# Kernel tuning notes

Measured on AMD Instinct MI355X. Metric: run time of the kernel, lower is better.

Reference implementation:

```python
import jax, jax.numpy as jnp
import numpy as np

B, L, DIM, H = 2, 2048, 3072, 24
D = DIM // H  # head_dim = 128
EPS = 1e-6


def _rms_norm(x, scale):
    # matches torch RMSNorm: compute in fp32, eps=1e-6, scale of shape [D]
    x32 = x.astype(jnp.float32)
    rrms = jax.lax.rsqrt(jnp.mean(x32 * x32, axis=-1, keepdims=True) + EPS)
    return (x32 * rrms * scale.astype(jnp.float32)).astype(x.dtype)


def _apply_rope(t, pe):
    # t: [B,H,L,D]; pe: [B,1,L,D//2,2,2]
    t_ = t.astype(jnp.float32).reshape(B, H, L, D // 2, 1, 2)
    out = pe[..., 0] * t_[..., 0] + pe[..., 1] * t_[..., 1]  # [B,H,L,D//2,2]
    return out.reshape(B, H, L, D).astype(t.dtype)


def setup_inputs() -> dict:
    key = jax.random.key(0)
    ks = jax.random.split(key, 7)
    x = jax.random.normal(ks[0], (B, L, DIM), jnp.float32)
    pe = jax.random.normal(ks[1], (B, 1, L, D // 2, 2, 2), jnp.float32)
    qkv_w = jax.random.normal(ks[2], (3 * DIM, DIM), jnp.float32) * (DIM ** -0.5)
    proj_w = jax.random.normal(ks[3], (DIM, DIM), jnp.float32) * (DIM ** -0.5)
    proj_b = jnp.zeros((DIM,), jnp.float32)
    q_scale = jnp.ones((D,), jnp.float32)
    k_scale = jnp.ones((D,), jnp.float32)
    return {"x": x, "pe": pe, "qkv_w": qkv_w, "proj_w": proj_w,
            "proj_b": proj_b, "q_scale": q_scale, "k_scale": k_scale}


def reference(x, pe, qkv_w, proj_w, proj_b, q_scale, k_scale):
    # fused QKV projection: [B,L,3*DIM]
    qkv = jnp.einsum('bld,ed->ble', x, qkv_w)
    # 'B L (K H D) -> K B H L D'
    qkv = qkv.reshape(B, L, 3, H, D).transpose(2, 0, 3, 1, 4)
    q, k, v = qkv[0], qkv[1], qkv[2]
    # QK-RMSNorm over head_dim
    q = _rms_norm(q, q_scale)
    k = _rms_norm(k, k_scale)
    # RoPE
    q = _apply_rope(q, pe)
    k = _apply_rope(k, pe)
    # scaled dot-product attention (no mask)
    scores = jnp.einsum('bhqd,bhkd->bhqk', q, k) / jnp.sqrt(jnp.float32(D))
    attn = jax.nn.softmax(scores, axis=-1)
    o = jnp.einsum('bhqk,bhkd->bhqd', attn, v)
    # 'B H L D -> B L (H D)'
    o = o.transpose(0, 2, 1, 3).reshape(B, L, DIM)
    return o @ proj_w.T + proj_b
```

## Files before the change

kernel.cpp:

```cpp
#include <hip/hip_runtime.h>

typedef unsigned short ushort_t;
typedef unsigned short ushort8 __attribute__((ext_vector_type(8)));
typedef __bf16 bf16x8 __attribute__((ext_vector_type(8)));
typedef float f32x4 __attribute__((ext_vector_type(4)));
typedef float f32x16 __attribute__((ext_vector_type(16)));
typedef unsigned uint32x4 __attribute__((ext_vector_type(4)));

#define DEV __device__ __forceinline__

DEV ushort_t f2bf(float f) {
  unsigned u = __builtin_bit_cast(unsigned, f);
  u += 0x7FFFu + ((u >> 16) & 1u);
  return (ushort_t)(u >> 16);
}
DEV float bf2f(ushort_t u) {
  return __builtin_bit_cast(float, ((unsigned)u) << 16);
}
DEV void gload_lds16(const void* g, void* s) {
  __builtin_amdgcn_global_load_lds(
      (__attribute__((address_space(1))) void*)(size_t)g,
      (__attribute__((address_space(3))) void*)(size_t)s, 16, 0, 0);
}
DEV f32x4 mfma_bf16(ushort8 a, ushort8 b, f32x4 c) {
  return __builtin_amdgcn_mfma_f32_16x16x32_bf16(
      __builtin_bit_cast(bf16x8, a), __builtin_bit_cast(bf16x8, b), c, 0, 0, 0);
}
DEV f32x16 mfma32(ushort8 a, ushort8 b, f32x16 c) {
  return __builtin_amdgcn_mfma_f32_32x32x16_bf16(
      __builtin_bit_cast(bf16x8, a), __builtin_bit_cast(bf16x8, b), c, 0, 0, 0);
}
DEV f32x16 zero16() {
  f32x16 z;
#pragma unroll
  for (int i = 0; i < 16; ++i) z[i] = 0.f;
  return z;
}
DEV unsigned cvtpk(float lo, float hi2) {
  unsigned r;
  asm("v_cvt_pk_bf16_f32 %0, %1, %2" : "=v"(r) : "v"(lo), "v"(hi2));
  return r;
}
DEV void swap32(unsigned &x, unsigned &y) {
#if __has_builtin(__builtin_amdgcn_permlane32_swap)
  auto t = __builtin_amdgcn_permlane32_swap(x, y, false, false);
  x = (unsigned)t[0];
  y = (unsigned)t[1];
#else
  unsigned xs = (unsigned)__shfl_xor((int)x, 32, 64);
  unsigned ys = (unsigned)__shfl_xor((int)y, 32, 64);
  bool h = (threadIdx.x & 63) >= 32;
  unsigned nx = h ? ys : x;
  unsigned ny = h ? y : xs;
  x = nx; y = ny;
#endif
}
DEV void barx() {
  asm volatile("" ::: "memory");
  __builtin_amdgcn_s_barrier();
  asm volatile("" ::: "memory");
}
#define GATE_VM2 asm volatile("s_waitcnt vmcnt(2)" ::: "memory")
#define GATE_VM8 asm volatile("s_waitcnt vmcnt(8)" ::: "memory")

__global__ void cast_bf16(const float4* __restrict__ in,
                          ushort4* __restrict__ out, int n4) {
  int stride = gridDim.x * blockDim.x;
  for (int i = blockIdx.x * blockDim.x + threadIdx.x; i < n4; i += stride) {
    float4 v = in[i];
    out[i] = make_ushort4(f2bf(v.x), f2bf(v.y), f2bf(v.z), f2bf(v.w));
  }
}

template <int OUT_BF16, int ADD_BIAS>
__global__ __launch_bounds__(512, 2)
void gemm256(const ushort_t* __restrict__ A, const ushort_t* __restrict__ Bw,
             const float* __restrict__ bias, void* __restrict__ Cp,
             int M, int N, int K) {
  __shared__ ushort_t As[2][256 * 64];
  __shared__ ushort_t Bs[2][256 * 64];
  const int tid = threadIdx.x;
  const int w = tid >> 6, l = tid & 63;
  const int g = l >> 4, r = l & 15;
  const int wm = w >> 2, wn = w & 3;
  const int m0 = blockIdx.y * 256, n0 = blockIdx.x * 256;
  const int NT = K >> 6;
  const int NI = NT >> 1;

  int srow[4], soff[4];
#pragma unroll
  for (int i = 0; i < 4; ++i) {
    int u = i * 512 + tid;
    int row = u >> 3, pc = u & 7;
    srow[i] = row;
    soff[i] = (pc ^ (row & 7)) * 8;
  }

  auto stA = [&](int i, int t, int db) {
    gload_lds16(A + (size_t)(m0 + srow[i]) * K + t * 64 + soff[i],
                As[db] + (i * 512 + w * 64) * 8);
  };
  auto stB = [&](int i, int t, int db) {
    gload_lds16(Bw + (size_t)(n0 + srow[i]) * K + t * 64 + soff[i],
                Bs[db] + (i * 512 + w * 64) * 8);
  };
  auto rdA = [&](int db, int mi, int kk) -> ushort8 {
    int row = wm * 128 + mi * 16 + r;
    return *(const ushort8*)(As[db] + row * 64 + (((kk << 2) + g) ^ (r & 7)) * 8);
  };
  auto rdB = [&](int db, int ni, int kk) -> ushort8 {
    int col = wn * 64 + ni * 16 + r;
    return *(const ushort8*)(Bs[db] + col * 64 + (((kk << 2) + g) ^ (r & 7)) * 8);
  };

  f32x4 acc[8][4];
#pragma unroll
  for (int i = 0; i < 8; ++i)
#pragma unroll
    for (int j = 0; j < 4; ++j) acc[i][j] = f32x4{0.f, 0.f, 0.f, 0.f};

  ushort8 af[4][2], bf[4][2];

  stA(0, 0, 0); stA(2, 0, 0);
  stB(0, 0, 0); stB(1, 0, 0); stB(2, 0, 0); stB(3, 0, 0);
  stA(1, 0, 0); stA(3, 0, 0);
  GATE_VM2;
  barx();

  for (int it = 0; it < NI; ++it) {
#pragma unroll
    for (int half = 0; half < 2; ++half) {
      const int db = half;
      int ts = 2 * it + 1 + half;
      if (ts > NT - 1) ts = NT - 1;

#pragma unroll
      for (int mi = 0; mi < 4; ++mi)
#pragma unroll
        for (int kk = 0; kk < 2; ++kk) af[mi][kk] = rdA(db, mi, kk);
#pragma unroll
      for (int ni = 0; ni < 2; ++ni)
#pragma unroll
        for (int kk = 0; kk < 2; ++kk) bf[ni][kk] = rdB(db, ni, kk);
      stA(0, ts, db ^ 1); stA(2, ts, db ^ 1);
      stB(0, ts, db ^ 1); stB(1, ts, db ^ 1);
      barx();
      __builtin_amdgcn_s_setprio(1);
#pragma unroll
      for (int mi = 0; mi < 4; ++mi)
#pragma unroll
        for (int ni = 0; ni < 2; ++ni)
#pragma unroll
          for (int kk = 0; kk < 2; ++kk)
            acc[mi][ni] = mfma_bf16(af[mi][kk], bf[ni][kk], acc[mi][ni]);
      __builtin_amdgcn_s_setprio(0);
      barx();

#pragma unroll
      for (int ni = 2; ni < 4; ++ni)
#pragma unroll
        for (int kk = 0; kk < 2; ++kk) bf[ni][kk] = rdB(db, ni, kk);
      stB(2, ts, db ^ 1); stB(3, ts, db ^ 1);
      stA(1, ts, db ^ 1); stA(3, ts, db ^ 1);
      barx();
      __builtin_amdgcn_s_setprio(1);
#pragma unroll
      for (int mi = 0; mi < 4; ++mi)
#pragma unroll
        for (int ni = 2; ni < 4; ++ni)
#pragma unroll
          for (int kk = 0; kk < 2; ++kk)
            acc[mi][ni] = mfma_bf16(af[mi][kk], bf[ni][kk], acc[mi][ni]);
      __builtin_amdgcn_s_setprio(0);
      GATE_VM8;
      barx();

#pragma unroll
      for (int mi = 0; mi < 4; ++mi)
#pragma unroll
        for (int kk = 0; kk < 2; ++kk) af[mi][kk] = rdA(db, mi + 4, kk);
      barx();
      __builtin_amdgcn_s_setprio(1);
#pragma unroll
      for (int mi = 0; mi < 4; ++mi)
#pragma unroll
        for (int ni = 0; ni < 2; ++ni)
#pragma unroll
          for (int kk = 0; kk < 2; ++kk)
            acc[mi + 4][ni] = mfma_bf16(af[mi][kk], bf[ni][kk], acc[mi + 4][ni]);
      __builtin_amdgcn_s_setprio(0);
      barx();

      __builtin_amdgcn_s_setprio(1);
#pragma unroll
      for (int mi = 0; mi < 4; ++mi)
#pragma unroll
        for (int ni = 2; ni < 4; ++ni)
#pragma unroll
          for (int kk = 0; kk < 2; ++kk)
            acc[mi + 4][ni] = mfma_bf16(af[mi][kk], bf[ni][kk], acc[mi + 4][ni]);
      __builtin_amdgcn_s_setprio(0);
      GATE_VM2;
      barx();
    }
  }

#pragma unroll
  for (int mi = 0; mi < 8; ++mi) {
#pragma unroll
    for (int ni = 0; ni < 4; ++ni) {
#pragma unroll
      for (int j = 0; j < 4; ++j) {
        int row = m0 + wm * 128 + mi * 16 + g * 4 + j;
        int col = n0 + wn * 64 + ni * 16 + r;
        float v = acc[mi][ni][j];
        if (ADD_BIAS) v += bias[col];
        if (OUT_BF16)
          ((ushort_t*)Cp)[(size_t)row * N + col] = f2bf(v);
        else
          ((float*)Cp)[(size_t)row * N + col] = v;
      }
    }
  }
}

__global__ __launch_bounds__(256)
void norm_rope(const ushort_t* __restrict__ qkv, const float* __restrict__ pe,
               const float* __restrict__ qs, const float* __restrict__ ksc,
               ushort_t* __restrict__ qb, ushort_t* __restrict__ kb,
               ushort_t* __restrict__ vtg) {
  __shared__ ushort_t Vt_lds[128 * 64];
  const int tid = threadIdx.x;
  const int w = tid >> 6, lane = tid & 63;
  const int tb = blockIdx.x, h = blockIdx.y;
  const int bl0 = tb * 64;
  const int b = bl0 >> 11, l0 = bl0 & 2047;
  const int i2 = lane * 2;

  const float sq0 = qs[i2], sq1 = qs[i2 + 1];
  const float sk0 = ksc[i2], sk1 = ksc[i2 + 1];
  const float QSC = 0.12751744f;

  for (int t = 0; t < 16; ++t) {
    const int bl = bl0 + w * 16 + t;
    const float4 p4 = *(const float4*)(pe + (size_t)bl * 256 + lane * 4);
    const size_t src = (size_t)bl * 9216 + h * 128 + i2;
    const size_t dst = ((size_t)(b * 24 + h) * 2048 + (bl & 2047)) * 128 + i2;
    {
      unsigned u = *(const unsigned*)(qkv + src);
      float x0 = bf2f((ushort_t)(u & 0xFFFFu)), x1 = bf2f((ushort_t)(u >> 16));
      float ss = x0 * x0 + x1 * x1;
#pragma unroll
      for (int mm = 32; mm; mm >>= 1) ss += __shfl_xor(ss, mm, 64);
      float rr = rsqrtf(ss * (1.f / 128.f) + 1e-6f);
      float y0 = x0 * rr * sq0, y1 = x1 * rr * sq1;
      float o0 = (p4.x * y0 + p4.y * y1) * QSC;
      float o1 = (p4.z * y0 + p4.w * y1) * QSC;
      *(unsigned*)(qb + dst) = (unsigned)f2bf(o0) | ((unsigned)f2bf(o1) << 16);
    }
    {
      unsigned u = *(const unsigned*)(qkv + src + 3072);
      float x0 = bf2f((ushort_t)(u & 0xFFFFu)), x1 = bf2f((ushort_t)(u >> 16));
      float ss = x0 * x0 + x1 * x1;
#pragma unroll
      for (int mm = 32; mm; mm >>= 1) ss += __shfl_xor(ss, mm, 64);
      float rr = rsqrtf(ss * (1.f / 128.f) + 1e-6f);
      float y0 = x0 * rr * sk0, y1 = x1 * rr * sk1;
      float o0 = p4.x * y0 + p4.y * y1;
      float o1 = p4.z * y0 + p4.w * y1;
      *(unsigned*)(kb + dst) = (unsigned)f2bf(o0) | ((unsigned)f2bf(o1) << 16);
    }
  }

  {
    const ushort_t* vsrc = qkv + (size_t)(bl0 + lane) * 9216 + 6144 + h * 128;
#pragma unroll
    for (int i = 0; i < 4; ++i) {
      int oct = w * 4 + i;
      ushort8 vv = *(const ushort8*)(vsrc + oct * 8);
#pragma unroll
      for (int j = 0; j < 8; ++j) {
        int d = oct * 8 + j;
        int ba = (d * 128 + lane * 2) ^ (j << 4);
        *(ushort_t*)((char*)Vt_lds + ba) = vv[j];
      }
    }
  }
  __syncthreads();

  {
    const int d = tid >> 1, half = tid & 1;
    ushort_t* orow = vtg + ((size_t)(b * 24 + h) * 128 + d) * 2048 + l0 + half * 32;
#pragma unroll
    for (int q = 0; q < 4; ++q) {
      int lb = d * 128 + half * 64 + q * 16;
      ushort8 vv = *(const ushort8*)((char*)Vt_lds + (lb ^ ((d & 7) << 4)));
      *(ushort8*)(orow + q * 8) = vv;
    }
  }
}

__global__ __launch_bounds__(256, 2)
void attn_fwd(const ushort_t* __restrict__ qb, const ushort_t* __restrict__ kb,
              const ushort_t* __restrict__ vt, ushort_t* __restrict__ ob) {
  __shared__ ushort_t Ks[64 * 128];
  __shared__ ushort_t Vts[128 * 64];
  const int tid = threadIdx.x;
  const int w = tid >> 6, l = tid & 63;
  const int c = l & 31, hi = l >> 5;
  const int bh = blockIdx.y;
  const int q0 = blockIdx.x * 128 + w * 32;

  const ushort_t* qrow = qb + ((size_t)bh * 2048 + q0 + c) * 128;
  ushort8 qf[8];
#pragma unroll
  for (int s = 0; s < 8; ++s)
    qf[s] = *(const ushort8*)(qrow + s * 16 + hi * 8);

  f32x16 o[4];
#pragma unroll
  for (int dt = 0; dt < 4; ++dt) o[dt] = zero16();
  float m = -1e30f, lp = 0.f;

  const ushort_t* kbase = kb + (size_t)bh * 2048 * 128;
  const ushort_t* vbase = vt + (size_t)bh * 128 * 2048;

  for (int kt = 0; kt < 2048; kt += 64) {
    __syncthreads();
#pragma unroll
    for (int i = 0; i < 4; ++i) {
      int u = w * 256 + i * 64 + l;
      int kr = u >> 4, kc = (u & 15) ^ (kr & 15);
      gload_lds16(kbase + (size_t)(kt + kr) * 128 + kc * 8,
                  Ks + (w * 256 + i * 64) * 8);
      int vr = u >> 3, vc = (u & 7) ^ (vr & 7);
      gload_lds16(vbase + (size_t)vr * 2048 + kt + vc * 8,
                  Vts + (w * 256 + i * 64) * 8);
    }
    __syncthreads();

    f32x16 s0 = zero16(), s1 = zero16();
#pragma unroll
    for (int ds = 0; ds < 8; ++ds) {
      int ch = (2 * ds + hi) ^ (c & 15);
      ushort8 k0 = *(const ushort8*)(Ks + c * 128 + ch * 8);
      ushort8 k1 = *(const ushort8*)(Ks + (32 + c) * 128 + ch * 8);
      s0 = mfma32(k0, qf[ds], s0);
      s1 = mfma32(k1, qf[ds], s1);
    }

    float p[32];
#pragma unroll
    for (int rr = 0; rr < 16; ++rr) { p[rr] = s0[rr]; p[16 + rr] = s1[rr]; }
    float pmax = p[0];
#pragma unroll
    for (int rr = 1; rr < 32; ++rr) pmax = fmaxf(pmax, p[rr]);
    if (!__all(pmax <= m + 8.f)) {
      float wm = pmax;
#pragma unroll
      for (int d = 1; d < 64; d <<= 1) wm = fmaxf(wm, __shfl_xor(wm, d, 64));
      float mn = fmaxf(m, wm);
      float fs = exp2f(m - mn);
      m = mn;
      lp *= fs;
#pragma unroll
      for (int dt = 0; dt < 4; ++dt)
#pragma unroll
        for (int e = 0; e < 16; ++e) o[dt][e] *= fs;
    }
    float rs = 0.f;
#pragma unroll
    for (int rr = 0; rr < 32; ++rr) { p[rr] = exp2f(p[rr] - m); rs += p[rr]; }
    lp += rs;

    uint32x4 pk[4];
#pragma unroll
    for (int ks = 0; ks < 4; ++ks) {
      unsigned a0 = cvtpk(p[ks * 8 + 0], p[ks * 8 + 1]);
      unsigned a1 = cvtpk(p[ks * 8 + 2], p[ks * 8 + 3]);
      unsigned a2 = cvtpk(p[ks * 8 + 4], p[ks * 8 + 5]);
      unsigned a3 = cvtpk(p[ks * 8 + 6], p[ks * 8 + 7]);
      swap32(a0, a2);
      swap32(a1, a3);
      pk[ks] = uint32x4{a0, a1, a2, a3};
    }

#pragma unroll
    for (int dt = 0; dt < 4; ++dt) {
#pragma unroll
      for (int ks = 0; ks < 4; ++ks) {
        int ch = (2 * ks + hi) ^ (c & 7);
        ushort8 vf = *(const ushort8*)(Vts + (32 * dt + c) * 64 + ch * 8);
        o[dt] = mfma32(__builtin_bit_cast(ushort8, pk[ks]), vf, o[dt]);
      }
    }
  }

  float lr = lp + __shfl_xor(lp, 32, 64);
  float rl = 1.f / lr;
  const int b = bh / 24, h = bh % 24;
  ushort_t* obase = ob + ((size_t)b * 2048 + q0) * 3072 + h * 128 + c;
#pragma unroll
  for (int rr = 0; rr < 16; ++rr) {
    int q = (rr & 3) + 8 * (rr >> 2) + 4 * hi;
    float os = __shfl(rl, q, 64);
#pragma unroll
    for (int dt = 0; dt < 4; ++dt)
      obase[(size_t)q * 3072 + dt * 32] = f2bf(o[dt][rr] * os);
  }
}

extern "C" void kernel_launch(void* const* d_in, const int* in_sizes, int n_in,
                              void* d_out, int out_size, void* d_ws, size_t ws_size,
                              hipStream_t stream) {
  const float* x    = (const float*)d_in[0];
  const float* pe   = (const float*)d_in[1];
  const float* qkvw = (const float*)d_in[2];
  const float* pw   = (const float*)d_in[3];
  const float* pb   = (const float*)d_in[4];
  const float* qsc  = (const float*)d_in[5];
  const float* ksc  = (const float*)d_in[6];
  float* out = (float*)d_out;

  char* p = (char*)d_ws;
  ushort_t* x_bf  = (ushort_t*)(p + 0);
  ushort_t* o_bf  = x_bf;
  ushort_t* qw_bf = (ushort_t*)(p + 25165824);
  ushort_t* pw_bf = (ushort_t*)(p + 81788928);
  ushort_t* qkv   = (ushort_t*)(p + 100663296);
  ushort_t* qh    = (ushort_t*)(p + 176160768);
  ushort_t* kh    = (ushort_t*)(p + 201326592);
  ushort_t* vtg   = (ushort_t*)(p + 226492416);

  cast_bf16<<<2048, 256, 0, stream>>>((const float4*)x,    (ushort4*)x_bf,  4096 * 3072 / 4);
  cast_bf16<<<2048, 256, 0, stream>>>((const float4*)qkvw, (ushort4*)qw_bf, 9216 * 3072 / 4);
  cast_bf16<<<2048, 256, 0, stream>>>((const float4*)pw,   (ushort4*)pw_bf, 3072 * 3072 / 4);

  gemm256<1, 0><<<dim3(36, 16), 512, 0, stream>>>(x_bf, qw_bf, nullptr, qkv, 4096, 9216, 3072);
  norm_rope<<<dim3(64, 24), 256, 0, stream>>>(qkv, pe, qsc, ksc, qh, kh, vtg);
  attn_fwd<<<dim3(16, 48), 256, 0, stream>>>(qh, kh, vtg, o_bf);
  gemm256<0, 1><<<dim3(12, 16), 512, 0, stream>>>(o_bf, pw_bf, pb, out, 4096, 3072, 3072);
}
```

Measured before the change: 562.4 us.

## Use 256x192 GEMM tiles with XCD-swizzled grid; double-buffer attention K/V

The GEMM moves from 256x256 to 256x192 output tiles, giving 768 and 256 workgroups, and remaps workgroup ids so consecutive blocks spread across the chiplets (XCDs). Its K-loop is restructured into one step per k-tile, with a two-tile-ahead prefetch of part of the tile gated by vmcnt(5). The attention kernel gains double-buffered K/V LDS tiles, so the next tile loads while the current one computes. It also swizzles block ids and raises wave priority around the MFMA sections. These changes target wave-quantization, L2 locality and exposed load latency, at the cost of more LDS in attention and more complex waitcnt reasoning.

```diff
diff --git a/kernel.cpp b/kernel.cpp
--- a/kernel.cpp
+++ b/kernel.cpp
@@ -60,7 +60,8 @@
   __builtin_amdgcn_s_barrier();
   asm volatile("" ::: "memory");
 }
-#define GATE_VM2 asm volatile("s_waitcnt vmcnt(2)" ::: "memory")
+#define GATE_VM0 asm volatile("s_waitcnt vmcnt(0)" ::: "memory")
+#define GATE_VM5 asm volatile("s_waitcnt vmcnt(5)" ::: "memory")
 #define GATE_VM8 asm volatile("s_waitcnt vmcnt(8)" ::: "memory")
 
 __global__ void cast_bf16(const float4* __restrict__ in,
@@ -74,145 +75,142 @@
 
 template <int OUT_BF16, int ADD_BIAS>
 __global__ __launch_bounds__(512, 2)
-void gemm256(const ushort_t* __restrict__ A, const ushort_t* __restrict__ Bw,
-             const float* __restrict__ bias, void* __restrict__ Cp,
-             int M, int N, int K) {
+void gemmT(const ushort_t* __restrict__ A, const ushort_t* __restrict__ Bw,
+           const float* __restrict__ bias, void* __restrict__ Cp,
+           int M, int N, int K) {
   __shared__ ushort_t As[2][256 * 64];
-  __shared__ ushort_t Bs[2][256 * 64];
+  __shared__ ushort_t Bs[2][192 * 64];
   const int tid = threadIdx.x;
   const int w = tid >> 6, l = tid & 63;
   const int g = l >> 4, r = l & 15;
   const int wm = w >> 2, wn = w & 3;
-  const int m0 = blockIdx.y * 256, n0 = blockIdx.x * 256;
+  const int gx = gridDim.x;
+  const int nwg = gx * gridDim.y;
+  const int id = blockIdx.y * gx + blockIdx.x;
+  const int swz = (id & 7) * (nwg >> 3) + (id >> 3);
+  const int m0 = (swz / gx) * 256, n0 = (swz % gx) * 192;
   const int NT = K >> 6;
-  const int NI = NT >> 1;
 
   int srow[4], soff[4];
 #pragma unroll
   for (int i = 0; i < 4; ++i) {
     int u = i * 512 + tid;
-    int row = u >> 3, pc = u & 7;
+    int row = u >> 3;
     srow[i] = row;
-    soff[i] = (pc ^ (row & 7)) * 8;
-  }
-
-  auto stA = [&](int i, int t, int db) {
+    soff[i] = ((u & 7) ^ (row & 7)) * 8;
+  }
+
+  auto stA = [&](int i, int t, int b) {
     gload_lds16(A + (size_t)(m0 + srow[i]) * K + t * 64 + soff[i],
-                As[db] + (i * 512 + w * 64) * 8);
+                As[b] + (i * 512 + w * 64) * 8);
   };
-  auto stB = [&](int i, int t, int db) {
+  auto stB = [&](int i, int t, int b) {
     gload_lds16(Bw + (size_t)(n0 + srow[i]) * K + t * 64 + soff[i],
-                Bs[db] + (i * 512 + w * 64) * 8);
+                Bs[b] + (i * 512 + w * 64) * 8);
   };
-  auto rdA = [&](int db, int mi, int kk) -> ushort8 {
+  auto rdA = [&](int b, int mi, int kk) -> ushort8 {
     int row = wm * 128 + mi * 16 + r;
-    return *(const ushort8*)(As[db] + row * 64 + (((kk << 2) + g) ^ (r & 7)) * 8);
+    return *(const ushort8*)(As[b] + row * 64 + (((kk << 2) + g) ^ (r & 7)) * 8);
   };
-  auto rdB = [&](int db, int ni, int kk) -> ushort8 {
-    int col = wn * 64 + ni * 16 + r;
-    return *(const ushort8*)(Bs[db] + col * 64 + (((kk << 2) + g) ^ (r & 7)) * 8);
+  auto rdB = [&](int b, int ni, int kk) -> ushort8 {
+    int col = wn * 48 + ni * 16 + r;
+    return *(const ushort8*)(Bs[b] + col * 64 + (((kk << 2) + g) ^ (r & 7)) * 8);
   };
 
-  f32x4 acc[8][4];
+  f32x4 acc[8][3];
 #pragma unroll
   for (int i = 0; i < 8; ++i)
 #pragma unroll
-    for (int j = 0; j < 4; ++j) acc[i][j] = f32x4{0.f, 0.f, 0.f, 0.f};
-
-  ushort8 af[4][2], bf[4][2];
+    for (int j = 0; j < 3; ++j) acc[i][j] = f32x4{0.f, 0.f, 0.f, 0.f};
+
+  ushort8 af[4][2], bf[3][2];
 
   stA(0, 0, 0); stA(2, 0, 0);
-  stB(0, 0, 0); stB(1, 0, 0); stB(2, 0, 0); stB(3, 0, 0);
+  stB(0, 0, 0); stB(1, 0, 0); stB(2, 0, 0);
   stA(1, 0, 0); stA(3, 0, 0);
-  GATE_VM2;
+  {
+    int t1 = (NT > 1) ? 1 : 0;
+    stA(0, t1, 1); stA(2, t1, 1);
+    stB(0, t1, 1); stB(1, t1, 1); stB(2, t1, 1);
+  }
+  GATE_VM5;
   barx();
 
-  for (int it = 0; it < NI; ++it) {
-#pragma unroll
-    for (int half = 0; half < 2; ++half) {
-      const int db = half;
-      int ts = 2 * it + 1 + half;
-      if (ts > NT - 1) ts = NT - 1;
-
-#pragma unroll
-      for (int mi = 0; mi < 4; ++mi)
-#pragma unroll
-        for (int kk = 0; kk < 2; ++kk) af[mi][kk] = rdA(db, mi, kk);
+  for (int t = 0; t < NT; ++t) {
+    const int db = t & 1;
+    const int ts1 = (t + 1 < NT) ? t + 1 : NT - 1;
+    const int ts2 = (t + 2 < NT) ? t + 2 : NT - 1;
+
+#pragma unroll
+    for (int mi = 0; mi < 4; ++mi)
+#pragma unroll
+      for (int kk = 0; kk < 2; ++kk) af[mi][kk] = rdA(db, mi, kk);
+#pragma unroll
+    for (int ni = 0; ni < 2; ++ni)
+#pragma unroll
+      for (int kk = 0; kk < 2; ++kk) bf[ni][kk] = rdB(db, ni, kk);
+    stA(1, ts1, db ^ 1); stA(3, ts1, db ^ 1);
+    barx();
+    __builtin_amdgcn_s_setprio(1);
+#pragma unroll
+    for (int mi = 0; mi < 4; ++mi)
 #pragma unroll
       for (int ni = 0; ni < 2; ++ni)
 #pragma unroll
-        for (int kk = 0; kk < 2; ++kk) bf[ni][kk] = rdB(db, ni, kk);
-      stA(0, ts, db ^ 1); stA(2, ts, db ^ 1);
-      stB(0, ts, db ^ 1); stB(1, ts, db ^ 1);
-      barx();
-      __builtin_amdgcn_s_setprio(1);
-#pragma unroll
-      for (int mi = 0; mi < 4; ++mi)
-#pragma unroll
-        for (int ni = 0; ni < 2; ++ni)
-#pragma unroll
-          for (int kk = 0; kk < 2; ++kk)
-            acc[mi][ni] = mfma_bf16(af[mi][kk], bf[ni][kk], acc[mi][ni]);
-      __builtin_amdgcn_s_setprio(0);
-      barx();
-
-#pragma unroll
-      for (int ni = 2; ni < 4; ++ni)
-#pragma unroll
-        for (int kk = 0; kk < 2; ++kk) bf[ni][kk] = rdB(db, ni, kk);
-      stB(2, ts, db ^ 1); stB(3, ts, db ^ 1);
-      stA(1, ts, db ^ 1); stA(3, ts, db ^ 1);
-      barx();
-      __builtin_amdgcn_s_setprio(1);
-#pragma unroll
-      for (int mi = 0; mi < 4; ++mi)
-#pragma unroll
-        for (int ni = 2; ni < 4; ++ni)
-#pragma unroll
-          for (int kk = 0; kk < 2; ++kk)
-            acc[mi][ni] = mfma_bf16(af[mi][kk], bf[ni][kk], acc[mi][ni]);
-      __builtin_amdgcn_s_setprio(0);
-      GATE_VM8;
-      barx();
-
-#pragma unroll
-      for (int mi = 0; mi < 4; ++mi)
-#pragma unroll
-        for (int kk = 0; kk < 2; ++kk) af[mi][kk] = rdA(db, mi + 4, kk);
-      barx();
-      __builtin_amdgcn_s_setprio(1);
-#pragma unroll
-      for (int mi = 0; mi < 4; ++mi)
-#pragma unroll
-        for (int ni = 0; ni < 2; ++ni)
-#pragma unroll
-          for (int kk = 0; kk < 2; ++kk)
-            acc[mi + 4][ni] = mfma_bf16(af[mi][kk], bf[ni][kk], acc[mi + 4][ni]);
-      __builtin_amdgcn_s_setprio(0);
-      barx();
-
-      __builtin_amdgcn_s_setprio(1);
-#pragma unroll
-      for (int mi = 0; mi < 4; ++mi)
-#pragma unroll
-        for (int ni = 2; ni < 4; ++ni)
-#pragma unroll
-          for (int kk = 0; kk < 2; ++kk)
-            acc[mi + 4][ni] = mfma_bf16(af[mi][kk], bf[ni][kk], acc[mi + 4][ni]);
-      __builtin_amdgcn_s_setprio(0);
-      GATE_VM2;
-      barx();
-    }
+        for (int kk = 0; kk < 2; ++kk)
+          acc[mi][ni] = mfma_bf16(af[mi][kk], bf[ni][kk], acc[mi][ni]);
+    __builtin_amdgcn_s_setprio(0);
+    barx();
+
+#pragma unroll
+    for (int kk = 0; kk < 2; ++kk) bf[2][kk] = rdB(db, 2, kk);
+    barx();
+    __builtin_amdgcn_s_setprio(1);
+#pragma unroll
+    for (int mi = 0; mi < 4; ++mi)
+#pragma unroll
+      for (int kk = 0; kk < 2; ++kk)
+        acc[mi][2] = mfma_bf16(af[mi][kk], bf[2][kk], acc[mi][2]);
+    __builtin_amdgcn_s_setprio(0);
+    barx();
+
+#pragma unroll
+    for (int mi = 0; mi < 4; ++mi)
+#pragma unroll
+      for (int kk = 0; kk < 2; ++kk) af[mi][kk] = rdA(db, mi + 4, kk);
+    barx();
+    __builtin_amdgcn_s_setprio(1);
+#pragma unroll
+    for (int mi = 0; mi < 4; ++mi)
+#pragma unroll
+      for (int ni = 0; ni < 2; ++ni)
+#pragma unroll
+        for (int kk = 0; kk < 2; ++kk)
+          acc[mi + 4][ni] = mfma_bf16(af[mi][kk], bf[ni][kk], acc[mi + 4][ni]);
+    __builtin_amdgcn_s_setprio(0);
+    barx();
+
+    stA(0, ts2, db); stA(2, ts2, db);
+    stB(0, ts2, db); stB(1, ts2, db); stB(2, ts2, db);
+    __builtin_amdgcn_s_setprio(1);
+#pragma unroll
+    for (int mi = 0; mi < 4; ++mi)
+#pragma unroll
+      for (int kk = 0; kk < 2; ++kk)
+        acc[mi + 4][2] = mfma_bf16(af[mi][kk], bf[2][kk], acc[mi + 4][2]);
+    __builtin_amdgcn_s_setprio(0);
+    GATE_VM5;
+    barx();
   }
 
 #pragma unroll
   for (int mi = 0; mi < 8; ++mi) {
 #pragma unroll
-    for (int ni = 0; ni < 4; ++ni) {
+    for (int ni = 0; ni < 3; ++ni) {
 #pragma unroll
       for (int j = 0; j < 4; ++j) {
         int row = m0 + wm * 128 + mi * 16 + g * 4 + j;
-        int col = n0 + wn * 64 + ni * 16 + r;
+        int col = n0 + wn * 48 + ni * 16 + r;
         float v = acc[mi][ni][j];
         if (ADD_BIAS) v += bias[col];
         if (OUT_BF16)
@@ -303,13 +301,15 @@
 __global__ __launch_bounds__(256, 2)
 void attn_fwd(const ushort_t* __restrict__ qb, const ushort_t* __restrict__ kb,
               const ushort_t* __restrict__ vt, ushort_t* __restrict__ ob) {
-  __shared__ ushort_t Ks[64 * 128];
-  __shared__ ushort_t Vts[128 * 64];
+  __shared__ ushort_t Ks[2][64 * 128];
+  __shared__ ushort_t Vts[2][128 * 64];
   const int tid = threadIdx.x;
   const int w = tid >> 6, l = tid & 63;
   const int c = l & 31, hi = l >> 5;
-  const int bh = blockIdx.y;
-  const int q0 = blockIdx.x * 128 + w * 32;
+  const int id = blockIdx.y * 16 + blockIdx.x;
+  const int swz = (id & 7) * 96 + (id >> 3);
+  const int bh = swz >> 4;
+  const int q0 = (swz & 15) * 128 + w * 32;
 
   const ushort_t* qrow = qb + ((size_t)bh * 2048 + q0 + c) * 128;
   ushort8 qf[8];
@@ -325,29 +325,42 @@
   const ushort_t* kbase = kb + (size_t)bh * 2048 * 128;
   const ushort_t* vbase = vt + (size_t)bh * 128 * 2048;
 
-  for (int kt = 0; kt < 2048; kt += 64) {
-    __syncthreads();
+  auto stage = [&](int t, int b) {
 #pragma unroll
     for (int i = 0; i < 4; ++i) {
       int u = w * 256 + i * 64 + l;
       int kr = u >> 4, kc = (u & 15) ^ (kr & 15);
-      gload_lds16(kbase + (size_t)(kt + kr) * 128 + kc * 8,
-                  Ks + (w * 256 + i * 64) * 8);
+      gload_lds16(kbase + (size_t)(t * 64 + kr) * 128 + kc * 8,
+                  Ks[b] + (w * 256 + i * 64) * 8);
       int vr = u >> 3, vc = (u & 7) ^ (vr & 7);
-      gload_lds16(vbase + (size_t)vr * 2048 + kt + vc * 8,
-                  Vts + (w * 256 + i * 64) * 8);
-    }
-    __syncthreads();
+      gload_lds16(vbase + (size_t)vr * 2048 + t * 64 + vc * 8,
+                  Vts[b] + (w * 256 + i * 64) * 8);
+    }
+  };
+
+  stage(0, 0);
+
+  for (int t = 0; t < 32; ++t) {
+    const int db = t & 1;
+    if (t < 31) {
+      stage(t + 1, db ^ 1);
+      GATE_VM8;
+    } else {
+      GATE_VM0;
+    }
+    barx();
 
     f32x16 s0 = zero16(), s1 = zero16();
+    __builtin_amdgcn_s_setprio(1);
 #pragma unroll
     for (int ds = 0; ds < 8; ++ds) {
       int ch = (2 * ds + hi) ^ (c & 15);
-      ushort8 k0 = *(const ushort8*)(Ks + c * 128 + ch * 8);
-      ushort8 k1 = *(const ushort8*)(Ks + (32 + c) * 128 + ch * 8);
+      ushort8 k0 = *(const ushort8*)(Ks[db] + c * 128 + ch * 8);
+      ushort8 k1 = *(const ushort8*)(Ks[db] + (32 + c) * 128 + ch * 8);
       s0 = mfma32(k0, qf[ds], s0);
       s1 = mfma32(k1, qf[ds], s1);
     }
+    __builtin_amdgcn_s_setprio(0);
 
     float p[32];
 #pragma unroll
@@ -385,15 +398,18 @@
       pk[ks] = uint32x4{a0, a1, a2, a3};
     }
 
+    __builtin_amdgcn_s_setprio(1);
 #pragma unroll
     for (int dt = 0; dt < 4; ++dt) {
 #pragma unroll
       for (int ks = 0; ks < 4; ++ks) {
         int ch = (2 * ks + hi) ^ (c & 7);
-        ushort8 vf = *(const ushort8*)(Vts + (32 * dt + c) * 64 + ch * 8);
+        ushort8 vf = *(const ushort8*)(Vts[db] + (32 * dt + c) * 64 + ch * 8);
         o[dt] = mfma32(__builtin_bit_cast(ushort8, pk[ks]), vf, o[dt]);
       }
     }
+    __builtin_amdgcn_s_setprio(0);
+    barx();
   }
 
   float lr = lp + __shfl_xor(lp, 32, 64);
@@ -436,8 +452,8 @@
   cast_bf16<<<2048, 256, 0, stream>>>((const float4*)qkvw, (ushort4*)qw_bf, 9216 * 3072 / 4);
   cast_bf16<<<2048, 256, 0, stream>>>((const float4*)pw,   (ushort4*)pw_bf, 3072 * 3072 / 4);
 
-  gemm256<1, 0><<<dim3(36, 16), 512, 0, stream>>>(x_bf, qw_bf, nullptr, qkv, 4096, 9216, 3072);
+  gemmT<1, 0><<<dim3(48, 16), 512, 0, stream>>>(x_bf, qw_bf, nullptr, qkv, 4096, 9216, 3072);
   norm_rope<<<dim3(64, 24), 256, 0, stream>>>(qkv, pe, qsc, ksc, qh, kh, vtg);
   attn_fwd<<<dim3(16, 48), 256, 0, stream>>>(qh, kh, vtg, o_bf);
-  gemm256<0, 1><<<dim3(12, 16), 512, 0, stream>>>(o_bf, pw_bf, pb, out, 4096, 3072, 3072);
-}
+  gemmT<0, 1><<<dim3(16, 16), 512, 0, stream>>>(o_bf, pw_bf, pb, out, 4096, 3072, 3072);
+}
```

Result: faster. 522.0 us (-7.2%).
